# Performance work log

Measured on AMD Instinct MI355X. Metric: run time of the kernel, lower is better.

The kernel has to match this reference:

```python
import jax, jax.numpy as jnp
import numpy as np

N_USERS = 4096
N_ITEMS = 8192
N_NODES = N_USERS + N_ITEMS
N_EDGES = 393216
D = 256
N_LAYERS = 3
MAX_TIME = 366
SLOPE = 0.2  # args.slope for LeakyReLU


def setup_inputs() -> dict:
    key = jax.random.key(0)
    ks = jax.random.split(key, 10)
    user_embd = jax.random.normal(ks[0], (N_USERS, D), jnp.float32) * 0.05
    item_embd = jax.random.normal(ks[1], (N_ITEMS, D), jnp.float32) * 0.05
    # interaction-weight parameters are initialized to ones in the original module
    w_p = jnp.ones((N_NODES, N_NODES), jnp.float32)
    w_n = jnp.ones((N_NODES, N_NODES), jnp.float32)
    layer_W = jax.random.normal(ks[2], (N_LAYERS, D, D), jnp.float32) * (1.0 / np.sqrt(D))
    time_table = jax.random.normal(ks[3], (MAX_TIME, D), jnp.float32) * 0.05
    # time-decayed positive/negative adjacency values (exp decay in (0,1])
    val_p = jax.random.uniform(ks[4], (N_EDGES,), jnp.float32)
    val_n = jax.random.uniform(ks[5], (N_EDGES,), jnp.float32)
    src = jax.random.randint(ks[6], (N_EDGES,), 0, N_NODES, dtype=jnp.int32)
    dst = jax.random.randint(ks[7], (N_EDGES,), 0, N_NODES, dtype=jnp.int32)
    time_idx = jax.random.randint(ks[8], (N_EDGES,), 0, MAX_TIME, dtype=jnp.int32)
    return {
        "user_embd": user_embd, "item_embd": item_embd,
        "w_p": w_p, "w_n": w_n, "layer_W": layer_W, "time_table": time_table,
        "val_p": val_p, "val_n": val_n,
        "src": src, "dst": dst, "time_idx": time_idx,
    }


def reference(user_embd, item_embd, w_p, w_n, layer_W, time_table,
              val_p, val_n, src, dst, time_idx):
    # weighted_pos_neg_matix: edge weight = T_p*w_p[src,dst] - T_n*w_n[src,dst]
    edge_w = val_p * w_p[src, dst] - val_n * w_n[src, dst]          # [E]
    # TimeEmbedding lookup per edge
    edge_feat = time_table[time_idx]                                 # [E, D]
    h = jnp.concatenate([user_embd, item_embd], axis=0)              # [N, D]
    embs = [h]  # layer-0 embeddings are kept unnormalized, as in the original
    for i in range(N_LAYERS):
        # GCNLayer: linear transform, weighted message passing over the
        # sparse graph with per-edge time features, LeakyReLU activation
        hw = h @ layer_W[i]                                          # [N, D]
        msg = (hw[src] + edge_feat) * edge_w[:, None]                # [E, D]
        agg = jax.ops.segment_sum(msg, dst, num_segments=N_NODES)   # [N, D]
        h = jax.nn.leaky_relu(agg, SLOPE)
        # F.normalize(p=2, dim=1) on the layer output; next layer consumes
        # the UN-normalized embeddings (matches the torch forward loop)
        norm = jnp.sqrt(jnp.sum(h * h, axis=1, keepdims=True))
        embs.append(h / jnp.maximum(norm, 1e-12))
    node_embedding = jnp.concatenate(embs, axis=1)                   # [N, (L+1)*D]
    # user_embedding = node_embedding[:N_USERS], item = node_embedding[N_USERS:]
    return node_embedding
```

## Files before the change

kernel.cpp:

```cpp
#include <hip/hip_runtime.h>

#define N_USERS  4096
#define N_NODES  12288
#define N_EDGES  393216
#define D        256
#define SLOPE    0.2f

__global__ void k_zero_counts(int* __restrict__ counts) {
    int i = blockIdx.x * blockDim.x + threadIdx.x;
    if (i < N_NODES) counts[i] = 0;
}

__global__ void k_hist(const int* __restrict__ dst, int* __restrict__ counts) {
    int e = blockIdx.x * blockDim.x + threadIdx.x;
    if (e < N_EDGES) atomicAdd(&counts[dst[e]], 1);
}

__global__ void k_scan(const int* __restrict__ counts, int* __restrict__ offs,
                       int* __restrict__ cursor) {
    __shared__ int buf[1024];
    __shared__ int carry_s;
    int t = threadIdx.x;
    if (t == 0) { carry_s = 0; offs[0] = 0; }
    __syncthreads();
    for (int base = 0; base < N_NODES; base += 1024) {
        int v = counts[base + t];
        buf[t] = v;
        __syncthreads();
        for (int off = 1; off < 1024; off <<= 1) {
            int add = (t >= off) ? buf[t - off] : 0;
            __syncthreads();
            buf[t] += add;
            __syncthreads();
        }
        int inc = buf[t] + carry_s;
        offs[base + t + 1] = inc;
        cursor[base + t] = inc - v;
        __syncthreads();
        if (t == 1023) carry_s = inc;
        __syncthreads();
    }
}

__global__ void k_scatter(const float* __restrict__ wp, const float* __restrict__ wn,
                          const float* __restrict__ valp, const float* __restrict__ valn,
                          const int* __restrict__ src, const int* __restrict__ dst,
                          const int* __restrict__ tix,
                          int* __restrict__ cursor,
                          int* __restrict__ e_src, float* __restrict__ e_w,
                          int* __restrict__ e_t) {
    int e = blockIdx.x * blockDim.x + threadIdx.x;
    if (e >= N_EDGES) return;
    int s = src[e], d0 = dst[e];
    size_t mi = (size_t)s * N_NODES + (size_t)d0;
    float w = valp[e] * wp[mi] - valn[e] * wn[mi];
    int pos = atomicAdd(&cursor[d0], 1);
    e_src[pos] = s;
    e_w[pos]   = w;
    e_t[pos]   = tix[e];
}

__global__ void k_build_B(const int* __restrict__ offs,
                          const float* __restrict__ e_w, const int* __restrict__ e_t,
                          const float* __restrict__ T, float* __restrict__ Bm) {
    int n = blockIdx.x;
    int d = threadIdx.x;
    int beg = offs[n], end = offs[n + 1];
    __shared__ float sw[256];
    __shared__ int   st[256];
    float acc = 0.f;
    for (int c = beg; c < end; c += 256) {
        int m = min(256, end - c);
        if (d < m) { sw[d] = e_w[c + d]; st[d] = e_t[c + d]; }
        __syncthreads();
        for (int j = 0; j < m; ++j)
            acc += sw[j] * T[st[j] * D + d];
        __syncthreads();
    }
    Bm[n * D + d] = acc;
}

__global__ void k_init_h(const float* __restrict__ user, const float* __restrict__ item,
                         float* __restrict__ h, float* __restrict__ out) {
    int idx = blockIdx.x * blockDim.x + threadIdx.x;
    int n = idx >> 8, d = idx & 255;
    float u = (n < N_USERS) ? user[n * D + d] : item[(n - N_USERS) * D + d];
    h[idx] = u;
    out[(size_t)n * (4 * D) + d] = u;
}

__global__ __launch_bounds__(256) void k_gemm(const float* __restrict__ h,
                                              const float* __restrict__ W,
                                              float* __restrict__ hw) {
    __shared__ float As[32 * 64];
    __shared__ float Bs[32 * 64];
    int tid = threadIdx.x;
    int tx = tid & 15, ty = tid >> 4;
    int row0 = blockIdx.x * 64, c0 = blockIdx.y * 64;
    float acc[4][4] = {};
    for (int k0 = 0; k0 < 256; k0 += 32) {
        {
            int r  = tid >> 2;
            int kq = (tid & 3) * 8;
            const float* s = &h[(row0 + r) * 256 + k0 + kq];
            float4 a0 = *(const float4*)s;
            float4 a1 = *(const float4*)(s + 4);
            As[(kq + 0) * 64 + r] = a0.x; As[(kq + 1) * 64 + r] = a0.y;
            As[(kq + 2) * 64 + r] = a0.z; As[(kq + 3) * 64 + r] = a0.w;
            As[(kq + 4) * 64 + r] = a1.x; As[(kq + 5) * 64 + r] = a1.y;
            As[(kq + 6) * 64 + r] = a1.z; As[(kq + 7) * 64 + r] = a1.w;
        }
        {
            int kb = tid >> 3;
            int c8 = (tid & 7) * 8;
            const float* ws = &W[(k0 + kb) * 256 + c0 + c8];
            float4 b0 = *(const float4*)ws;
            float4 b1 = *(const float4*)(ws + 4);
            float* bd = &Bs[kb * 64 + c8];
            bd[0] = b0.x; bd[1] = b0.y; bd[2] = b0.z; bd[3] = b0.w;
            bd[4] = b1.x; bd[5] = b1.y; bd[6] = b1.z; bd[7] = b1.w;
        }
        __syncthreads();
#pragma unroll
        for (int kk = 0; kk < 32; ++kk) {
            float4 a = *(const float4*)&As[kk * 64 + ty * 4];
            float4 b = *(const float4*)&Bs[kk * 64 + tx * 4];
            acc[0][0] += a.x * b.x; acc[0][1] += a.x * b.y; acc[0][2] += a.x * b.z; acc[0][3] += a.x * b.w;
            acc[1][0] += a.y * b.x; acc[1][1] += a.y * b.y; acc[1][2] += a.y * b.z; acc[1][3] += a.y * b.w;
            acc[2][0] += a.z * b.x; acc[2][1] += a.z * b.y; acc[2][2] += a.z * b.z; acc[2][3] += a.z * b.w;
            acc[3][0] += a.w * b.x; acc[3][1] += a.w * b.y; acc[3][2] += a.w * b.z; acc[3][3] += a.w * b.w;
        }
        __syncthreads();
    }
#pragma unroll
    for (int i = 0; i < 4; ++i) {
        float4 o;
        o.x = acc[i][0]; o.y = acc[i][1]; o.z = acc[i][2]; o.w = acc[i][3];
        *(float4*)&hw[(row0 + ty * 4 + i) * 256 + c0 + tx * 4] = o;
    }
}

__global__ void k_agg(const int* __restrict__ offs,
                      const int* __restrict__ e_src, const float* __restrict__ e_w,
                      const float* __restrict__ hw, const float* __restrict__ Bm,
                      float* __restrict__ h, float* __restrict__ out, int layer) {
    int n = blockIdx.x, d = threadIdx.x;
    int beg = offs[n], end = offs[n + 1];
    __shared__ float sw[256];
    __shared__ int   ss[256];
    float acc = Bm[n * D + d];
    for (int c = beg; c < end; c += 256) {
        int m = min(256, end - c);
        if (d < m) { sw[d] = e_w[c + d]; ss[d] = e_src[c + d]; }
        __syncthreads();
        for (int j = 0; j < m; ++j)
            acc += sw[j] * hw[ss[j] * D + d];
        __syncthreads();
    }
    float v = (acc >= 0.f) ? acc : SLOPE * acc;
    h[n * D + d] = v;
    float sq = v * v;
#pragma unroll
    for (int off = 32; off > 0; off >>= 1) sq += __shfl_down(sq, off, 64);
    __shared__ float red[4];
    int lane = d & 63, wv = d >> 6;
    if (lane == 0) red[wv] = sq;
    __syncthreads();
    float tot = red[0] + red[1] + red[2] + red[3];
    float scale = 1.0f / fmaxf(sqrtf(tot), 1e-12f);
    out[(size_t)n * (4 * D) + (size_t)(layer + 1) * D + d] = v * scale;
}

extern "C" void kernel_launch(void* const* d_in, const int* in_sizes, int n_in,
                              void* d_out, int out_size, void* d_ws, size_t ws_size,
                              hipStream_t stream) {
    const float* user  = (const float*)d_in[0];
    const float* item  = (const float*)d_in[1];
    const float* wp    = (const float*)d_in[2];
    const float* wn    = (const float*)d_in[3];
    const float* layW  = (const float*)d_in[4];
    const float* ttab  = (const float*)d_in[5];
    const float* valp  = (const float*)d_in[6];
    const float* valn  = (const float*)d_in[7];
    const int*   src   = (const int*)d_in[8];
    const int*   dst   = (const int*)d_in[9];
    const int*   tix   = (const int*)d_in[10];
    float* out = (float*)d_out;

    char* p = (char*)d_ws;
    auto carve = [&](size_t bytes) {
        char* r = p;
        p += (bytes + 255) & ~(size_t)255;
        return r;
    };
    int*   counts = (int*)  carve((size_t)N_NODES * 4);
    int*   offs   = (int*)  carve((size_t)(N_NODES + 1) * 4);
    int*   cursor = (int*)  carve((size_t)N_NODES * 4);
    int*   e_src  = (int*)  carve((size_t)N_EDGES * 4);
    float* e_w    = (float*)carve((size_t)N_EDGES * 4);
    int*   e_t    = (int*)  carve((size_t)N_EDGES * 4);
    float* Bm     = (float*)carve((size_t)N_NODES * D * 4);
    float* h      = (float*)carve((size_t)N_NODES * D * 4);
    float* hw     = (float*)carve((size_t)N_NODES * D * 4);

    k_zero_counts<<<(N_NODES + 255) / 256, 256, 0, stream>>>(counts);
    k_hist<<<N_EDGES / 256, 256, 0, stream>>>(dst, counts);
    k_scan<<<1, 1024, 0, stream>>>(counts, offs, cursor);
    k_scatter<<<N_EDGES / 256, 256, 0, stream>>>(wp, wn, valp, valn, src, dst, tix,
                                                 cursor, e_src, e_w, e_t);
    k_build_B<<<N_NODES, 256, 0, stream>>>(offs, e_w, e_t, ttab, Bm);
    k_init_h<<<N_NODES, 256, 0, stream>>>(user, item, h, out);

    for (int l = 0; l < 3; ++l) {
        k_gemm<<<dim3(N_NODES / 64, 4), 256, 0, stream>>>(h, layW + (size_t)l * 256 * 256, hw);
        k_agg<<<N_NODES, 256, 0, stream>>>(offs, e_src, e_w, hw, Bm, h, out, l);
    }
}
```

Baseline: 1.241 ms.

## Map one wavefront per node with float4 gathers in CSR aggregation kernels

Rewrites k_build_B and k_agg so each 64-lane wavefront handles one destination node, each lane owning four features via float4 loads. Edge indices and weights are broadcast with wave shuffles instead of shared memory and block barriers, with four edges processed per step to expose more memory-level parallelism. The L2-norm reduction becomes a single wave xor-shuffle with no shared memory. The aim is fewer barriers, wider loads and less per-block overhead. Because nodes have unequal degree, wavefronts in the same block may finish at different times.

Result: no change. 1.217 ms (-1.9%).

```diff
diff --git a/kernel.cpp b/kernel.cpp
--- a/kernel.cpp
+++ b/kernel.cpp
@@ -60,24 +60,42 @@
     e_t[pos]   = tix[e];
 }
 
-__global__ void k_build_B(const int* __restrict__ offs,
+__global__ __launch_bounds__(256) void k_build_B(const int* __restrict__ offs,
                           const float* __restrict__ e_w, const int* __restrict__ e_t,
                           const float* __restrict__ T, float* __restrict__ Bm) {
-    int n = blockIdx.x;
-    int d = threadIdx.x;
+    int wv = threadIdx.x >> 6, lane = threadIdx.x & 63;
+    int n = blockIdx.x * 4 + wv;
     int beg = offs[n], end = offs[n + 1];
-    __shared__ float sw[256];
-    __shared__ int   st[256];
-    float acc = 0.f;
-    for (int c = beg; c < end; c += 256) {
-        int m = min(256, end - c);
-        if (d < m) { sw[d] = e_w[c + d]; st[d] = e_t[c + d]; }
-        __syncthreads();
-        for (int j = 0; j < m; ++j)
-            acc += sw[j] * T[st[j] * D + d];
-        __syncthreads();
-    }
-    Bm[n * D + d] = acc;
+    const float4* T4 = (const float4*)T;
+    float4 acc = make_float4(0.f, 0.f, 0.f, 0.f);
+    for (int c = beg; c < end; c += 64) {
+        int idx = c + lane;
+        int   te = (idx < end) ? e_t[idx] : 0;
+        float we = (idx < end) ? e_w[idx] : 0.f;
+        int m = min(64, end - c);
+        int j = 0;
+        for (; j + 4 <= m; j += 4) {
+            int   t0 = __shfl(te, j),     t1 = __shfl(te, j + 1),
+                  t2 = __shfl(te, j + 2), t3 = __shfl(te, j + 3);
+            float w0 = __shfl(we, j),     w1 = __shfl(we, j + 1),
+                  w2 = __shfl(we, j + 2), w3 = __shfl(we, j + 3);
+            float4 r0 = T4[t0 * 64 + lane];
+            float4 r1 = T4[t1 * 64 + lane];
+            float4 r2 = T4[t2 * 64 + lane];
+            float4 r3 = T4[t3 * 64 + lane];
+            acc.x += w0 * r0.x + w1 * r1.x + w2 * r2.x + w3 * r3.x;
+            acc.y += w0 * r0.y + w1 * r1.y + w2 * r2.y + w3 * r3.y;
+            acc.z += w0 * r0.z + w1 * r1.z + w2 * r2.z + w3 * r3.z;
+            acc.w += w0 * r0.w + w1 * r1.w + w2 * r2.w + w3 * r3.w;
+        }
+        for (; j < m; ++j) {
+            int t0 = __shfl(te, j); float w0 = __shfl(we, j);
+            float4 r0 = T4[t0 * 64 + lane];
+            acc.x += w0 * r0.x; acc.y += w0 * r0.y;
+            acc.z += w0 * r0.z; acc.w += w0 * r0.w;
+        }
+    }
+    ((float4*)Bm)[n * 64 + lane] = acc;
 }
 
 __global__ void k_init_h(const float* __restrict__ user, const float* __restrict__ item,
@@ -140,35 +158,54 @@
     }
 }
 
-__global__ void k_agg(const int* __restrict__ offs,
+__global__ __launch_bounds__(256) void k_agg(const int* __restrict__ offs,
                       const int* __restrict__ e_src, const float* __restrict__ e_w,
                       const float* __restrict__ hw, const float* __restrict__ Bm,
                       float* __restrict__ h, float* __restrict__ out, int layer) {
-    int n = blockIdx.x, d = threadIdx.x;
+    int wv = threadIdx.x >> 6, lane = threadIdx.x & 63;
+    int n = blockIdx.x * 4 + wv;
     int beg = offs[n], end = offs[n + 1];
-    __shared__ float sw[256];
-    __shared__ int   ss[256];
-    float acc = Bm[n * D + d];
-    for (int c = beg; c < end; c += 256) {
-        int m = min(256, end - c);
-        if (d < m) { sw[d] = e_w[c + d]; ss[d] = e_src[c + d]; }
-        __syncthreads();
-        for (int j = 0; j < m; ++j)
-            acc += sw[j] * hw[ss[j] * D + d];
-        __syncthreads();
-    }
-    float v = (acc >= 0.f) ? acc : SLOPE * acc;
-    h[n * D + d] = v;
-    float sq = v * v;
+    const float4* hw4 = (const float4*)hw;
+    float4 acc = ((const float4*)Bm)[n * 64 + lane];
+    for (int c = beg; c < end; c += 64) {
+        int idx = c + lane;
+        int   se = (idx < end) ? e_src[idx] : 0;
+        float we = (idx < end) ? e_w[idx] : 0.f;
+        int m = min(64, end - c);
+        int j = 0;
+        for (; j + 4 <= m; j += 4) {
+            int   s0 = __shfl(se, j),     s1 = __shfl(se, j + 1),
+                  s2 = __shfl(se, j + 2), s3 = __shfl(se, j + 3);
+            float w0 = __shfl(we, j),     w1 = __shfl(we, j + 1),
+                  w2 = __shfl(we, j + 2), w3 = __shfl(we, j + 3);
+            float4 r0 = hw4[s0 * 64 + lane];
+            float4 r1 = hw4[s1 * 64 + lane];
+            float4 r2 = hw4[s2 * 64 + lane];
+            float4 r3 = hw4[s3 * 64 + lane];
+            acc.x += w0 * r0.x + w1 * r1.x + w2 * r2.x + w3 * r3.x;
+            acc.y += w0 * r0.y + w1 * r1.y + w2 * r2.y + w3 * r3.y;
+            acc.z += w0 * r0.z + w1 * r1.z + w2 * r2.z + w3 * r3.z;
+            acc.w += w0 * r0.w + w1 * r1.w + w2 * r2.w + w3 * r3.w;
+        }
+        for (; j < m; ++j) {
+            int s0 = __shfl(se, j); float w0 = __shfl(we, j);
+            float4 r0 = hw4[s0 * 64 + lane];
+            acc.x += w0 * r0.x; acc.y += w0 * r0.y;
+            acc.z += w0 * r0.z; acc.w += w0 * r0.w;
+        }
+    }
+    float4 v;
+    v.x = (acc.x >= 0.f) ? acc.x : SLOPE * acc.x;
+    v.y = (acc.y >= 0.f) ? acc.y : SLOPE * acc.y;
+    v.z = (acc.z >= 0.f) ? acc.z : SLOPE * acc.z;
+    v.w = (acc.w >= 0.f) ? acc.w : SLOPE * acc.w;
+    ((float4*)h)[n * 64 + lane] = v;
+    float sq = v.x * v.x + v.y * v.y + v.z * v.z + v.w * v.w;
 #pragma unroll
-    for (int off = 32; off > 0; off >>= 1) sq += __shfl_down(sq, off, 64);
-    __shared__ float red[4];
-    int lane = d & 63, wv = d >> 6;
-    if (lane == 0) red[wv] = sq;
-    __syncthreads();
-    float tot = red[0] + red[1] + red[2] + red[3];
-    float scale = 1.0f / fmaxf(sqrtf(tot), 1e-12f);
-    out[(size_t)n * (4 * D) + (size_t)(layer + 1) * D + d] = v * scale;
+    for (int off = 1; off < 64; off <<= 1) sq += __shfl_xor(sq, off, 64);
+    float scale = 1.0f / fmaxf(sqrtf(sq), 1e-12f);
+    float4 o = make_float4(v.x * scale, v.y * scale, v.z * scale, v.w * scale);
+    ((float4*)out)[(size_t)n * 256 + (size_t)(layer + 1) * 64 + lane] = o;
 }
 
 extern "C" void kernel_launch(void* const* d_in, const int* in_sizes, int n_in,
@@ -208,11 +245,11 @@
     k_scan<<<1, 1024, 0, stream>>>(counts, offs, cursor);
     k_scatter<<<N_EDGES / 256, 256, 0, stream>>>(wp, wn, valp, valn, src, dst, tix,
                                                  cursor, e_src, e_w, e_t);
-    k_build_B<<<N_NODES, 256, 0, stream>>>(offs, e_w, e_t, ttab, Bm);
+    k_build_B<<<N_NODES / 4, 256, 0, stream>>>(offs, e_w, e_t, ttab, Bm);
     k_init_h<<<N_NODES, 256, 0, stream>>>(user, item, h, out);
 
     for (int l = 0; l < 3; ++l) {
         k_gemm<<<dim3(N_NODES / 64, 4), 256, 0, stream>>>(h, layW + (size_t)l * 256 * 256, hw);
-        k_agg<<<N_NODES, 256, 0, stream>>>(offs, e_src, e_w, hw, Bm, h, out, l);
-    }
-}
+        k_agg<<<N_NODES / 4, 256, 0, stream>>>(offs, e_src, e_w, hw, Bm, h, out, l);
+    }
+}
```
